# Performance work log

Hardware: AMD Instinct MI355X
Metric: run time of the kernel (lower is better)

Reference implementation:

```python
import jax, jax.numpy as jnp
import numpy as np

N_NODES = 50000
N_EDGES = 640000
IN_CH, HID_CH, OUT_CH = 128, 128, 40


def setup_inputs() -> dict:
    key = jax.random.key(0)
    k1, k2, k3, k4 = jax.random.split(key, 4)
    x = jax.random.normal(k1, (N_NODES, IN_CH), dtype=jnp.float32)
    edge_index = jax.random.randint(k2, (2, N_EDGES), 0, N_NODES, dtype=jnp.int64)
    # Glorot-ish scaled weights
    W1 = jax.random.normal(k3, (IN_CH, HID_CH), dtype=jnp.float32) * (1.0 / np.sqrt(IN_CH))
    b1 = jnp.zeros((HID_CH,), dtype=jnp.float32)
    W2 = jax.random.normal(k4, (HID_CH, OUT_CH), dtype=jnp.float32) * (1.0 / np.sqrt(HID_CH))
    b2 = jnp.zeros((OUT_CH,), dtype=jnp.float32)
    return {"x": x, "edge_index": edge_index, "W1": W1, "b1": b1, "W2": W2, "b2": b2}


def gcn_conv(x, src, dst, W, b, n_nodes):
    """PyG-style GCNConv: self-loops + symmetric normalization + linear + bias.
    src/dst already include self-loop edges."""
    deg = jax.ops.segment_sum(jnp.ones_like(dst, dtype=x.dtype), dst, num_segments=n_nodes)
    dinv = jnp.where(deg > 0, jax.lax.rsqrt(deg), 0.0)          # deg^{-1/2}, 0 for isolated
    norm = dinv[src] * dinv[dst]                                 # [E+N]
    xw = x @ W                                                   # [N, F_out] dense GEMM
    msgs = xw[src] * norm[:, None]                               # gather + scale  [E+N, F_out]
    agg = jax.ops.segment_sum(msgs, dst, num_segments=n_nodes)   # scatter-add
    return agg + b


def reference(x, edge_index, W1, b1, W2, b2):
    n_nodes = x.shape[0]
    loops = jnp.arange(n_nodes, dtype=edge_index.dtype)
    src = jnp.concatenate([edge_index[0], loops])
    dst = jnp.concatenate([edge_index[1], loops])
    h = jax.nn.relu(gcn_conv(x, src, dst, W1, b1, n_nodes))
    # dropout is identity in eval mode (deterministic reference)
    return gcn_conv(h, src, dst, W2, b2, n_nodes)
```

## Files before the change

kernel.cpp:

```cpp
#include <hip/hip_runtime.h>
#include <cstdint>

#define NN 50000
#define NE 640000

typedef unsigned short ushort_t;

__device__ __forceinline__ ushort_t f2bf(float f) {
    unsigned int b = __float_as_uint(f);
    return (ushort_t)((b + 0x7FFF + ((b >> 16) & 1)) >> 16);
}
__device__ __forceinline__ float bf2f(ushort_t u) {
    return __uint_as_float(((unsigned int)u) << 16);
}


__global__ void hist_kernel(const int* __restrict__ dst, int* __restrict__ cnt) {
    int tid = blockIdx.x * 256 + threadIdx.x;
#pragma unroll
    for (int k = 0; k < 4; ++k) {
        int e = tid + k * 160000;
        atomicAdd(&cnt[dst[e]], 1);
    }
}

__global__ void scan_block(const int* __restrict__ in, int* __restrict__ out,
                           int* __restrict__ partials, int n) {
    __shared__ int sm[256];
    int t = threadIdx.x;
    int gid = blockIdx.x * 256 + t;
    int v = (gid < n) ? in[gid] : 0;
    sm[t] = v;
    __syncthreads();
#pragma unroll
    for (int off = 1; off < 256; off <<= 1) {
        int add = (t >= off) ? sm[t - off] : 0;
        __syncthreads();
        sm[t] += add;
        __syncthreads();
    }
    if (gid < n) out[gid] = sm[t] - v;
    if (t == 255) partials[blockIdx.x] = sm[255];
}

__global__ void scan_partials(int* __restrict__ p, int nb) {
    __shared__ int sm[256];
    int t = threadIdx.x;
    int v = (t < nb) ? p[t] : 0;
    sm[t] = v;
    __syncthreads();
#pragma unroll
    for (int off = 1; off < 256; off <<= 1) {
        int add = (t >= off) ? sm[t - off] : 0;
        __syncthreads();
        sm[t] += add;
        __syncthreads();
    }
    if (t < nb) p[t] = sm[t] - v;
}

__global__ void finalize_offsets(int* __restrict__ offs, const int* __restrict__ partials,
                                 int* __restrict__ cursor, const int* __restrict__ cnt,
                                 float* __restrict__ dinv, int n) {
    int gid = blockIdx.x * 256 + threadIdx.x;
    if (gid < n) {
        int v = offs[gid] + partials[blockIdx.x];
        offs[gid] = v;
        cursor[gid] = v;
        dinv[gid] = rsqrtf((float)cnt[gid] + 1.0f);
    }
}

__global__ void csr_fill(const int* __restrict__ ei, int* __restrict__ cursor,
                         int* __restrict__ csr_src) {
    int tid = blockIdx.x * 256 + threadIdx.x;
#pragma unroll
    for (int k = 0; k < 4; ++k) {
        int e = tid + k * 160000;
        int s = ei[e], d = ei[NE + e];
        int pos = atomicAdd(&cursor[d], 1);
        csr_src[pos] = s;
    }
}


__global__ __launch_bounds__(256) void gemm_k128_scaled(const float* __restrict__ A,
                                                        const float* __restrict__ B,
                                                        const float* __restrict__ dinv,
                                                        ushort_t* __restrict__ C,
                                                        int M, int N) {
    __shared__ float As[64][68];
    __shared__ __align__(16) float Bs[64][64];
    const int t  = threadIdx.x;
    const int m0 = blockIdx.x * 64;
    const int n0 = blockIdx.y * 64;
    const int tx = t & 15, ty = t >> 4;

    float acc[4][4] = {};

    for (int ks = 0; ks < 2; ++ks) {
#pragma unroll
        for (int i = 0; i < 4; ++i) {
            int idx = i * 256 + t;
            int r = idx >> 4, c4 = idx & 15;
            int gm = m0 + r;
            float4 v = make_float4(0.f, 0.f, 0.f, 0.f);
            if (gm < M) v = *reinterpret_cast<const float4*>(&A[(size_t)gm * 128 + ks * 64 + c4 * 4]);
            As[r][c4 * 4 + 0] = v.x;
            As[r][c4 * 4 + 1] = v.y;
            As[r][c4 * 4 + 2] = v.z;
            As[r][c4 * 4 + 3] = v.w;
        }
#pragma unroll
        for (int i = 0; i < 4; ++i) {
            int idx = i * 256 + t;
            int k = idx >> 4, c4 = idx & 15;
            int gk = ks * 64 + k;
            int gn = n0 + c4 * 4;
            float4 v;
            v.x = (gn + 0 < N) ? B[(size_t)gk * N + gn + 0] : 0.f;
            v.y = (gn + 1 < N) ? B[(size_t)gk * N + gn + 1] : 0.f;
            v.z = (gn + 2 < N) ? B[(size_t)gk * N + gn + 2] : 0.f;
            v.w = (gn + 3 < N) ? B[(size_t)gk * N + gn + 3] : 0.f;
            *reinterpret_cast<float4*>(&Bs[k][c4 * 4]) = v;
        }
        __syncthreads();

#pragma unroll 8
        for (int k = 0; k < 64; ++k) {
            float a0 = As[ty * 4 + 0][k];
            float a1 = As[ty * 4 + 1][k];
            float a2 = As[ty * 4 + 2][k];
            float a3 = As[ty * 4 + 3][k];
            float4 b = *reinterpret_cast<const float4*>(&Bs[k][tx * 4]);
            acc[0][0] += a0 * b.x; acc[0][1] += a0 * b.y; acc[0][2] += a0 * b.z; acc[0][3] += a0 * b.w;
            acc[1][0] += a1 * b.x; acc[1][1] += a1 * b.y; acc[1][2] += a1 * b.z; acc[1][3] += a1 * b.w;
            acc[2][0] += a2 * b.x; acc[2][1] += a2 * b.y; acc[2][2] += a2 * b.z; acc[2][3] += a2 * b.w;
            acc[3][0] += a3 * b.x; acc[3][1] += a3 * b.y; acc[3][2] += a3 * b.z; acc[3][3] += a3 * b.w;
        }
        __syncthreads();
    }

#pragma unroll
    for (int i = 0; i < 4; ++i) {
        int gm = m0 + ty * 4 + i;
        if (gm >= M) continue;
        float s = dinv[gm];
        int gn = n0 + tx * 4;
        if (gn + 3 < N) {
            ushort4 o;
            o.x = f2bf(acc[i][0] * s); o.y = f2bf(acc[i][1] * s);
            o.z = f2bf(acc[i][2] * s); o.w = f2bf(acc[i][3] * s);
            *reinterpret_cast<ushort4*>(&C[(size_t)gm * N + gn]) = o;
        } else {
#pragma unroll
            for (int j = 0; j < 4; ++j)
                if (gn + j < N) C[(size_t)gm * N + gn + j] = f2bf(acc[i][j] * s);
        }
    }
}


__global__ __launch_bounds__(256) void gather128(const int* __restrict__ offs,
                                                 const int* __restrict__ ends,
                                                 const int* __restrict__ csr_src,
                                                 const ushort_t* __restrict__ Hs,
                                                 const float* __restrict__ dinv,
                                                 const float* __restrict__ b1,
                                                 float* __restrict__ h) {
    const int c = (threadIdx.x & 31) * 4;
    const int n = (blockIdx.x * 256 + threadIdx.x) >> 5;
    const int beg = offs[n], end = ends[n];
    float4 acc = make_float4(0.f, 0.f, 0.f, 0.f);
    int j = beg;
    const int n4end = beg + ((end - beg) & ~3);
    for (; j < n4end; j += 4) {
        int s0 = csr_src[j + 0], s1 = csr_src[j + 1];
        int s2 = csr_src[j + 2], s3 = csr_src[j + 3];
        ushort4 v0 = *reinterpret_cast<const ushort4*>(Hs + (size_t)s0 * 128 + c);
        ushort4 v1 = *reinterpret_cast<const ushort4*>(Hs + (size_t)s1 * 128 + c);
        ushort4 v2 = *reinterpret_cast<const ushort4*>(Hs + (size_t)s2 * 128 + c);
        ushort4 v3 = *reinterpret_cast<const ushort4*>(Hs + (size_t)s3 * 128 + c);
        acc.x += bf2f(v0.x) + bf2f(v1.x) + bf2f(v2.x) + bf2f(v3.x);
        acc.y += bf2f(v0.y) + bf2f(v1.y) + bf2f(v2.y) + bf2f(v3.y);
        acc.z += bf2f(v0.z) + bf2f(v1.z) + bf2f(v2.z) + bf2f(v3.z);
        acc.w += bf2f(v0.w) + bf2f(v1.w) + bf2f(v2.w) + bf2f(v3.w);
    }
    for (; j < end; ++j) {
        int s = csr_src[j];
        ushort4 v = *reinterpret_cast<const ushort4*>(Hs + (size_t)s * 128 + c);
        acc.x += bf2f(v.x); acc.y += bf2f(v.y);
        acc.z += bf2f(v.z); acc.w += bf2f(v.w);
    }
    float di = dinv[n];
    ushort4 sv = *reinterpret_cast<const ushort4*>(Hs + (size_t)n * 128 + c);
    float4 bv = *reinterpret_cast<const float4*>(b1 + c);
    float4 r;
    r.x = fmaxf(fmaf(di, acc.x + bf2f(sv.x), bv.x), 0.f);
    r.y = fmaxf(fmaf(di, acc.y + bf2f(sv.y), bv.y), 0.f);
    r.z = fmaxf(fmaf(di, acc.z + bf2f(sv.z), bv.z), 0.f);
    r.w = fmaxf(fmaf(di, acc.w + bf2f(sv.w), bv.w), 0.f);
    *reinterpret_cast<float4*>(h + (size_t)n * 128 + c) = r;
}


__global__ __launch_bounds__(256) void gather40(const int* __restrict__ offs,
                                                const int* __restrict__ ends,
                                                const int* __restrict__ csr_src,
                                                const ushort_t* __restrict__ Hs,
                                                const float* __restrict__ dinv,
                                                const float* __restrict__ b2,
                                                float* __restrict__ out) {
    int idx = blockIdx.x * 256 + threadIdx.x;
    if (idx >= NN * 10) return;
    const int n = idx / 10;
    const int c = (idx - n * 10) * 4;
    const int beg = offs[n], end = ends[n];
    float4 acc = make_float4(0.f, 0.f, 0.f, 0.f);
    int j = beg;
    const int n4end = beg + ((end - beg) & ~3);
    for (; j < n4end; j += 4) {
        int s0 = csr_src[j + 0], s1 = csr_src[j + 1];
        int s2 = csr_src[j + 2], s3 = csr_src[j + 3];
        ushort4 v0 = *reinterpret_cast<const ushort4*>(Hs + (size_t)s0 * 40 + c);
        ushort4 v1 = *reinterpret_cast<const ushort4*>(Hs + (size_t)s1 * 40 + c);
        ushort4 v2 = *reinterpret_cast<const ushort4*>(Hs + (size_t)s2 * 40 + c);
        ushort4 v3 = *reinterpret_cast<const ushort4*>(Hs + (size_t)s3 * 40 + c);
        acc.x += bf2f(v0.x) + bf2f(v1.x) + bf2f(v2.x) + bf2f(v3.x);
        acc.y += bf2f(v0.y) + bf2f(v1.y) + bf2f(v2.y) + bf2f(v3.y);
        acc.z += bf2f(v0.z) + bf2f(v1.z) + bf2f(v2.z) + bf2f(v3.z);
        acc.w += bf2f(v0.w) + bf2f(v1.w) + bf2f(v2.w) + bf2f(v3.w);
    }
    for (; j < end; ++j) {
        int s = csr_src[j];
        ushort4 v = *reinterpret_cast<const ushort4*>(Hs + (size_t)s * 40 + c);
        acc.x += bf2f(v.x); acc.y += bf2f(v.y);
        acc.z += bf2f(v.z); acc.w += bf2f(v.w);
    }
    float di = dinv[n];
    ushort4 sv = *reinterpret_cast<const ushort4*>(Hs + (size_t)n * 40 + c);
    float4 bv = *reinterpret_cast<const float4*>(b2 + c);
    float4 r;
    r.x = fmaf(di, acc.x + bf2f(sv.x), bv.x);
    r.y = fmaf(di, acc.y + bf2f(sv.y), bv.y);
    r.z = fmaf(di, acc.z + bf2f(sv.z), bv.z);
    r.w = fmaf(di, acc.w + bf2f(sv.w), bv.w);
    *reinterpret_cast<float4*>(out + (size_t)n * 40 + c) = r;
}


extern "C" void kernel_launch(void* const* d_in, const int* in_sizes, int n_in,
                              void* d_out, int out_size, void* d_ws, size_t ws_size,
                              hipStream_t stream) {
    const float* x  = (const float*)d_in[0];
    const int*   ei = (const int*)d_in[1];
    const float* W1 = (const float*)d_in[2];
    const float* b1 = (const float*)d_in[3];
    const float* W2 = (const float*)d_in[4];
    const float* b2 = (const float*)d_in[5];
    float* out = (float*)d_out;

    int*      deg_i    = (int*)d_ws;
    float*    dinv     = (float*)d_ws + 50048;
    int*      offs     = (int*)d_ws + 100096;
    int*      cursor   = (int*)d_ws + 150144;
    int*      partials = (int*)d_ws + 200192;
    int*      csr_src  = (int*)d_ws + 200704;
    ushort_t* H1b      = (ushort_t*)((int*)d_ws + 840704);
    float*    h        = (float*)d_ws + 4040704;
    ushort_t* H2b      = H1b;

    const int NB = (NN + 255) / 256;

    hipMemsetAsync(deg_i, 0, NN * sizeof(int), stream);
    hist_kernel<<<625, 256, 0, stream>>>(ei + NE, deg_i);
    scan_block<<<NB, 256, 0, stream>>>(deg_i, offs, partials, NN);
    scan_partials<<<1, 256, 0, stream>>>(partials, NB);
    finalize_offsets<<<NB, 256, 0, stream>>>(offs, partials, cursor, deg_i, dinv, NN);
    csr_fill<<<625, 256, 0, stream>>>(ei, cursor, csr_src);

    gemm_k128_scaled<<<dim3((NN + 63) / 64, 2), 256, 0, stream>>>(x, W1, dinv, H1b, NN, 128);
    gather128<<<NN * 32 / 256, 256, 0, stream>>>(offs, cursor, csr_src, H1b, dinv, b1, h);

    gemm_k128_scaled<<<dim3((NN + 63) / 64, 1), 256, 0, stream>>>(h, W2, dinv, H2b, NN, 40);
    gather40<<<(NN * 10 + 255) / 256, 256, 0, stream>>>(offs, cursor, csr_src, H2b, dinv, b2, out);
}
```

Measured before the change: 244.8 us.

## Fuse CSR fill into first GEMM launch and store CSR indices as 16-bit

Measured after the change: 230.4 us. -5.9%, faster.

```diff
diff --git a/kernel.cpp b/kernel.cpp
--- a/kernel.cpp
+++ b/kernel.cpp
@@ -3,6 +3,8 @@
 
 #define NN 50000
 #define NE 640000
+#define NFILL 625
+#define MB1 782
 
 typedef unsigned short ushort_t;
 
@@ -71,15 +73,97 @@
     }
 }
 
-__global__ void csr_fill(const int* __restrict__ ei, int* __restrict__ cursor,
-                         int* __restrict__ csr_src) {
-    int tid = blockIdx.x * 256 + threadIdx.x;
-#pragma unroll
-    for (int k = 0; k < 4; ++k) {
-        int e = tid + k * 160000;
-        int s = ei[e], d = ei[NE + e];
-        int pos = atomicAdd(&cursor[d], 1);
-        csr_src[pos] = s;
+
+__global__ __launch_bounds__(256) void fused_fill_gemm(const int* __restrict__ ei,
+                                                       int* __restrict__ cursor,
+                                                       ushort_t* __restrict__ csr_src,
+                                                       const float* __restrict__ A,
+                                                       const float* __restrict__ B,
+                                                       const float* __restrict__ dinv,
+                                                       ushort_t* __restrict__ C,
+                                                       int M, int N) {
+    __shared__ float As[64][68];
+    __shared__ __align__(16) float Bs[64][64];
+
+    if (blockIdx.x < NFILL) {
+        int tid = blockIdx.x * 256 + threadIdx.x;
+#pragma unroll
+        for (int k = 0; k < 4; ++k) {
+            int e = tid + k * 160000;
+            int s = ei[e], d = ei[NE + e];
+            int pos = atomicAdd(&cursor[d], 1);
+            csr_src[pos] = (ushort_t)s;
+        }
+        return;
+    }
+
+    const int b  = blockIdx.x - NFILL;
+    const int t  = threadIdx.x;
+    const int m0 = (b % MB1) * 64;
+    const int n0 = (b / MB1) * 64;
+    const int tx = t & 15, ty = t >> 4;
+
+    float acc[4][4] = {};
+
+    for (int ks = 0; ks < 2; ++ks) {
+#pragma unroll
+        for (int i = 0; i < 4; ++i) {
+            int idx = i * 256 + t;
+            int r = idx >> 4, c4 = idx & 15;
+            int gm = m0 + r;
+            float4 v = make_float4(0.f, 0.f, 0.f, 0.f);
+            if (gm < M) v = *reinterpret_cast<const float4*>(&A[(size_t)gm * 128 + ks * 64 + c4 * 4]);
+            As[r][c4 * 4 + 0] = v.x;
+            As[r][c4 * 4 + 1] = v.y;
+            As[r][c4 * 4 + 2] = v.z;
+            As[r][c4 * 4 + 3] = v.w;
+        }
+#pragma unroll
+        for (int i = 0; i < 4; ++i) {
+            int idx = i * 256 + t;
+            int k = idx >> 4, c4 = idx & 15;
+            int gk = ks * 64 + k;
+            int gn = n0 + c4 * 4;
+            float4 v;
+            v.x = (gn + 0 < N) ? B[(size_t)gk * N + gn + 0] : 0.f;
+            v.y = (gn + 1 < N) ? B[(size_t)gk * N + gn + 1] : 0.f;
+            v.z = (gn + 2 < N) ? B[(size_t)gk * N + gn + 2] : 0.f;
+            v.w = (gn + 3 < N) ? B[(size_t)gk * N + gn + 3] : 0.f;
+            *reinterpret_cast<float4*>(&Bs[k][c4 * 4]) = v;
+        }
+        __syncthreads();
+
+#pragma unroll 8
+        for (int k = 0; k < 64; ++k) {
+            float a0 = As[ty * 4 + 0][k];
+            float a1 = As[ty * 4 + 1][k];
+            float a2 = As[ty * 4 + 2][k];
+            float a3 = As[ty * 4 + 3][k];
+            float4 bb = *reinterpret_cast<const float4*>(&Bs[k][tx * 4]);
+            acc[0][0] += a0 * bb.x; acc[0][1] += a0 * bb.y; acc[0][2] += a0 * bb.z; acc[0][3] += a0 * bb.w;
+            acc[1][0] += a1 * bb.x; acc[1][1] += a1 * bb.y; acc[1][2] += a1 * bb.z; acc[1][3] += a1 * bb.w;
+            acc[2][0] += a2 * bb.x; acc[2][1] += a2 * bb.y; acc[2][2] += a2 * bb.z; acc[2][3] += a2 * bb.w;
+            acc[3][0] += a3 * bb.x; acc[3][1] += a3 * bb.y; acc[3][2] += a3 * bb.z; acc[3][3] += a3 * bb.w;
+        }
+        __syncthreads();
+    }
+
+#pragma unroll
+    for (int i = 0; i < 4; ++i) {
+        int gm = m0 + ty * 4 + i;
+        if (gm >= M) continue;
+        float s = dinv[gm];
+        int gn = n0 + tx * 4;
+        if (gn + 3 < N) {
+            ushort4 o;
+            o.x = f2bf(acc[i][0] * s); o.y = f2bf(acc[i][1] * s);
+            o.z = f2bf(acc[i][2] * s); o.w = f2bf(acc[i][3] * s);
+            *reinterpret_cast<ushort4*>(&C[(size_t)gm * N + gn]) = o;
+        } else {
+#pragma unroll
+            for (int j = 0; j < 4; ++j)
+                if (gn + j < N) C[(size_t)gm * N + gn + j] = f2bf(acc[i][j] * s);
+        }
     }
 }
 
@@ -132,11 +216,11 @@
             float a1 = As[ty * 4 + 1][k];
             float a2 = As[ty * 4 + 2][k];
             float a3 = As[ty * 4 + 3][k];
-            float4 b = *reinterpret_cast<const float4*>(&Bs[k][tx * 4]);
-            acc[0][0] += a0 * b.x; acc[0][1] += a0 * b.y; acc[0][2] += a0 * b.z; acc[0][3] += a0 * b.w;
-            acc[1][0] += a1 * b.x; acc[1][1] += a1 * b.y; acc[1][2] += a1 * b.z; acc[1][3] += a1 * b.w;
-            acc[2][0] += a2 * b.x; acc[2][1] += a2 * b.y; acc[2][2] += a2 * b.z; acc[2][3] += a2 * b.w;
-            acc[3][0] += a3 * b.x; acc[3][1] += a3 * b.y; acc[3][2] += a3 * b.z; acc[3][3] += a3 * b.w;
+            float4 bb = *reinterpret_cast<const float4*>(&Bs[k][tx * 4]);
+            acc[0][0] += a0 * bb.x; acc[0][1] += a0 * bb.y; acc[0][2] += a0 * bb.z; acc[0][3] += a0 * bb.w;
+            acc[1][0] += a1 * bb.x; acc[1][1] += a1 * bb.y; acc[1][2] += a1 * bb.z; acc[1][3] += a1 * bb.w;
+            acc[2][0] += a2 * bb.x; acc[2][1] += a2 * bb.y; acc[2][2] += a2 * bb.z; acc[2][3] += a2 * bb.w;
+            acc[3][0] += a3 * bb.x; acc[3][1] += a3 * bb.y; acc[3][2] += a3 * bb.z; acc[3][3] += a3 * bb.w;
         }
         __syncthreads();
     }
@@ -163,7 +247,7 @@
 
 __global__ __launch_bounds__(256) void gather128(const int* __restrict__ offs,
                                                  const int* __restrict__ ends,
-                                                 const int* __restrict__ csr_src,
+                                                 const ushort_t* __restrict__ csr_src,
                                                  const ushort_t* __restrict__ Hs,
                                                  const float* __restrict__ dinv,
                                                  const float* __restrict__ b1,
@@ -206,7 +290,7 @@
 
 __global__ __launch_bounds__(256) void gather40(const int* __restrict__ offs,
                                                 const int* __restrict__ ends,
-                                                const int* __restrict__ csr_src,
+                                                const ushort_t* __restrict__ csr_src,
                                                 const ushort_t* __restrict__ Hs,
                                                 const float* __restrict__ dinv,
                                                 const float* __restrict__ b2,
@@ -265,9 +349,9 @@
     int*      offs     = (int*)d_ws + 100096;
     int*      cursor   = (int*)d_ws + 150144;
     int*      partials = (int*)d_ws + 200192;
-    int*      csr_src  = (int*)d_ws + 200704;
-    ushort_t* H1b      = (ushort_t*)((int*)d_ws + 840704);
-    float*    h        = (float*)d_ws + 4040704;
+    ushort_t* csr_src  = (ushort_t*)((int*)d_ws + 200704);
+    ushort_t* H1b      = (ushort_t*)((int*)d_ws + 520704);
+    float*    h        = (float*)d_ws + 3720704;
     ushort_t* H2b      = H1b;
 
     const int NB = (NN + 255) / 256;
@@ -277,11 +361,12 @@
     scan_block<<<NB, 256, 0, stream>>>(deg_i, offs, partials, NN);
     scan_partials<<<1, 256, 0, stream>>>(partials, NB);
     finalize_offsets<<<NB, 256, 0, stream>>>(offs, partials, cursor, deg_i, dinv, NN);
-    csr_fill<<<625, 256, 0, stream>>>(ei, cursor, csr_src);
-
-    gemm_k128_scaled<<<dim3((NN + 63) / 64, 2), 256, 0, stream>>>(x, W1, dinv, H1b, NN, 128);
+
+    fused_fill_gemm<<<NFILL + MB1 * 2, 256, 0, stream>>>(ei, cursor, csr_src,
+                                                         x, W1, dinv, H1b, NN, 128);
+
     gather128<<<NN * 32 / 256, 256, 0, stream>>>(offs, cursor, csr_src, H1b, dinv, b1, h);
 
-    gemm_k128_scaled<<<dim3((NN + 63) / 64, 1), 256, 0, stream>>>(h, W2, dinv, H2b, NN, 40);
+    gemm_k128_scaled<<<dim3(MB1, 1), 256, 0, stream>>>(h, W2, dinv, H2b, NN, 40);
     gather40<<<(NN * 10 + 255) / 256, 256, 0, stream>>>(offs, cursor, csr_src, H2b, dinv, b2, out);
 }
```
